# Optimization experiments

Measured on AMD Instinct MI355X. Metric: run time of the kernel, lower is better.

The kernel has to match this reference:

```python
import jax, jax.numpy as jnp
import numpy as np

B, T, D, H = 2, 2048, 1024, 16
Hd = D // H


def setup_inputs() -> dict:
    key = jax.random.key(0)
    ks = jax.random.split(key, 9)
    s = 1.0 / np.sqrt(D)
    return {
        "x": jax.random.normal(ks[0], (B, T, D), jnp.float32),
        "Wq": jax.random.normal(ks[1], (D, D), jnp.float32) * s,
        "bq": jax.random.normal(ks[2], (D,), jnp.float32) * 0.01,
        "Wk": jax.random.normal(ks[3], (D, D), jnp.float32) * s,
        "bk": jax.random.normal(ks[4], (D,), jnp.float32) * 0.01,
        "Wv": jax.random.normal(ks[5], (D, D), jnp.float32) * s,
        "bv": jax.random.normal(ks[6], (D,), jnp.float32) * 0.01,
        "Wo": jax.random.normal(ks[7], (D, D), jnp.float32) * s,
        "bo": jax.random.normal(ks[8], (D,), jnp.float32) * 0.01,
    }


def reference(x, Wq, bq, Wk, bk, Wv, bv, Wo, bo):
    # torch Linear: y = x @ W.T + b
    def proj(W, b):
        y = jnp.einsum('btd,ed->bte', x, W) + b          # [B,T,D]
        return y.reshape(B, T, H, Hd).transpose(0, 2, 1, 3)  # [B,H,T,Hd]
    q = proj(Wq, bq) / jnp.sqrt(jnp.asarray(Hd, x.dtype))
    k = proj(Wk, bk)
    v = proj(Wv, bv)
    scores = jnp.einsum('bhqd,bhkd->bhqk', q, k)         # [B,H,T,T]
    attn = jax.nn.softmax(scores, axis=-1)
    out = jnp.einsum('bhqk,bhkd->bhqd', attn, v)         # [B,H,T,Hd]
    out = out.transpose(0, 2, 1, 3).reshape(B, T, D)
    return jnp.einsum('btd,ed->bte', out, Wo) + bo
```

## Files before the change

kernel.cpp:

```cpp
#include <hip/hip_runtime.h>
#include <cmath>

typedef __attribute__((ext_vector_type(8))) short bf16x8;
typedef __attribute__((ext_vector_type(4))) float f32x4;

#define MFMA_BF16 __builtin_amdgcn_mfma_f32_16x16x32_bf16

__device__ __forceinline__ unsigned short f2b(float f) {
  union { float f; unsigned u; } v; v.f = f;
  unsigned r = (v.u + 0x7FFFu + ((v.u >> 16) & 1u)) >> 16;
  return (unsigned short)r;
}

__device__ __forceinline__ unsigned cvt_pk_bf16(float lo, float hi) {
  unsigned r;
  asm("v_cvt_pk_bf16_f32 %0, %1, %2" : "=v"(r) : "v"(lo), "v"(hi));
  return r;
}

__device__ __forceinline__ float fast_exp2(float x) {
  float r;
  asm("v_exp_f32 %0, %1" : "=v"(r) : "v"(x));
  return r;
}

__device__ __forceinline__ void gload_lds16(const void* g, void* l) {
  __builtin_amdgcn_global_load_lds(
      (const __attribute__((address_space(1))) void*)g,
      (__attribute__((address_space(3))) void*)l, 16, 0, 0);
}

__global__ __launch_bounds__(256) void cvt_all(
    const float* __restrict__ x, const float* __restrict__ Wq,
    const float* __restrict__ Wk, const float* __restrict__ Wv,
    const float* __restrict__ Wo,
    unsigned short* __restrict__ xb, unsigned short* __restrict__ wqb,
    unsigned short* __restrict__ wkb, unsigned short* __restrict__ wvb,
    unsigned short* __restrict__ wob) {
  int i = blockIdx.x * 256 + threadIdx.x;
  const float* src; unsigned short* dst; int off;
  if (i < 1048576)      { src = x;  dst = xb;  off = i; }
  else if (i < 1310720) { src = Wq; dst = wqb; off = i - 1048576; }
  else if (i < 1572864) { src = Wk; dst = wkb; off = i - 1310720; }
  else if (i < 1835008) { src = Wv; dst = wvb; off = i - 1572864; }
  else                  { src = Wo; dst = wob; off = i - 1835008; }
  float4 v = reinterpret_cast<const float4*>(src)[off];
  ushort4 o;
  o.x = f2b(v.x); o.y = f2b(v.y); o.z = f2b(v.z); o.w = f2b(v.w);
  reinterpret_cast<ushort4*>(dst)[off] = o;
}

__global__ __launch_bounds__(512, 4) void qkv_gemm(
    const unsigned short* __restrict__ X,
    const unsigned short* __restrict__ Wq, const unsigned short* __restrict__ Wk,
    const unsigned short* __restrict__ Wv,
    const float* __restrict__ bq, const float* __restrict__ bk,
    const float* __restrict__ bv,
    unsigned short* __restrict__ Qo, unsigned short* __restrict__ Ko,
    unsigned short* __restrict__ Vto) {
  __shared__ char smA[2][16384];
  __shared__ char smB[2][16384];
  const int tid = threadIdx.x, lane = tid & 63, wvid = tid >> 6;
  const int g = lane >> 4, l15 = lane & 15;
  const int wr = wvid >> 1, wc = wvid & 1;
  const int lin = blockIdx.y * 32 + blockIdx.x;
  const int xcd = lin & 7, j = lin >> 3;
  const int m_tile = (xcd >> 1) * 8 + (j & 7);
  const int bnall = (xcd & 1) * 12 + (j >> 3);
  const int m0 = m_tile * 128;
  const int wsel = bnall >> 3;
  const int n0 = (bnall & 7) * 128;
  const unsigned short* W = (wsel == 0) ? Wq : (wsel == 1) ? Wk : Wv;
  const float* bias = (wsel == 0) ? bq : (wsel == 1) ? bk : bv;

  f32x4 acc[2][4];
#pragma unroll
  for (int i = 0; i < 2; ++i)
#pragma unroll
    for (int j2 = 0; j2 < 4; ++j2) acc[i][j2] = (f32x4){0.f, 0.f, 0.f, 0.f};

#define QSTAGE(b, kt)                                                          \
  {                                                                            \
    _Pragma("unroll") for (int i = 0; i < 2; ++i) {                            \
      int c = (i * 8 + wvid) * 64 + lane;                                      \
      int row = c >> 3;                                                        \
      int cb = (c & 7) ^ (row & 7);                                            \
      gload_lds16(X + (size_t)(m0 + row) * 1024 + (kt) * 64 + cb * 8,          \
                  smA[b] + (i * 8 + wvid) * 1024);                             \
      gload_lds16(W + (size_t)(n0 + row) * 1024 + (kt) * 64 + cb * 8,          \
                  smB[b] + (i * 8 + wvid) * 1024);                             \
    }                                                                          \
  }

  QSTAGE(0, 0);
  int buf = 0;
  for (int kt = 0; kt < 16; ++kt) {
    __syncthreads();
    if (kt < 15) QSTAGE(buf ^ 1, kt + 1);
    bf16x8 af[2][2], bfr[4][2];
#pragma unroll
    for (int mi = 0; mi < 2; ++mi)
#pragma unroll
      for (int ks = 0; ks < 2; ++ks) {
        int rowa = wr * 32 + mi * 16 + l15;
        int addra = (rowa * 128 + ks * 64 + g * 16) ^ ((rowa & 7) << 4);
        af[mi][ks] = *(const bf16x8*)(smA[buf] + addra);
      }
#pragma unroll
    for (int ni = 0; ni < 4; ++ni)
#pragma unroll
      for (int ks = 0; ks < 2; ++ks) {
        int rowb = wc * 64 + ni * 16 + l15;
        int addrb = (rowb * 128 + ks * 64 + g * 16) ^ ((rowb & 7) << 4);
        bfr[ni][ks] = *(const bf16x8*)(smB[buf] + addrb);
      }
    __builtin_amdgcn_s_setprio(1);
#pragma unroll
    for (int ks = 0; ks < 2; ++ks)
#pragma unroll
      for (int mi = 0; mi < 2; ++mi)
#pragma unroll
        for (int ni = 0; ni < 4; ++ni)
          acc[mi][ni] = MFMA_BF16(af[mi][ks], bfr[ni][ks], acc[mi][ni], 0, 0, 0);
    __builtin_amdgcn_s_setprio(0);
    buf ^= 1;
  }

  const float qscale = (wsel == 0) ? 0.125f * 1.44269504f : 1.0f;
#pragma unroll
  for (int mi = 0; mi < 2; ++mi)
#pragma unroll
    for (int ni = 0; ni < 4; ++ni)
#pragma unroll
      for (int r = 0; r < 4; ++r) {
        int m = m0 + wr * 32 + mi * 16 + g * 4 + r;
        int n = n0 + wc * 64 + ni * 16 + l15;
        float v = (acc[mi][ni][r] + bias[n]) * qscale;
        int b = m >> 11, t = m & 2047;
        int h = n >> 6, hd = n & 63;
        unsigned short bv16 = f2b(v);
        if (wsel == 2)
          Vto[(((size_t)b * 16 + h) * 64 + hd) * 2048 + t] = bv16;
        else if (wsel == 1)
          Ko[(((size_t)b * 16 + h) * 2048 + t) * 64 + hd] = bv16;
        else
          Qo[(((size_t)b * 16 + h) * 2048 + t) * 64 + hd] = bv16;
      }
}

__global__ __launch_bounds__(512) void attn_kernel(
    const unsigned short* __restrict__ Qg, const unsigned short* __restrict__ Kg,
    const unsigned short* __restrict__ Vtg, unsigned short* __restrict__ Og) {
  __shared__ char smK[2][8192];
  __shared__ char smV[2][8192];
  __shared__ char smPT[8][2048];
  const int tid = threadIdx.x, lane = tid & 63, wvid = tid >> 6;
  const int g = lane >> 4, l15 = lane & 15;
  const int lin = blockIdx.y * 16 + blockIdx.x;
  const int wg = (lin & 7) * 64 + (lin >> 3);
  const int bx = wg & 15, bh = wg >> 4;
  const int q0 = bx * 128 + wvid * 16;
  const unsigned short* Qh = Qg + (size_t)bh * 2048 * 64;
  const unsigned short* Kh = Kg + (size_t)bh * 2048 * 64;
  const unsigned short* Vh = Vtg + (size_t)bh * 64 * 2048;

  bf16x8 qf[2];
#pragma unroll
  for (int ks = 0; ks < 2; ++ks)
    qf[ks] = *(const bf16x8*)(Qh + (size_t)(q0 + l15) * 64 + ks * 32 + g * 8);

  bf16x8 ones;
#pragma unroll
  for (int j = 0; j < 8; ++j) ones[j] = (short)0x3F80;

  f32x4 acc[4];
  f32x4 accL;
#pragma unroll
  for (int di = 0; di < 4; ++di) acc[di] = (f32x4){0.f, 0.f, 0.f, 0.f};
  accL = (f32x4){0.f, 0.f, 0.f, 0.f};
  float m = -1e30f;

#define STAGE(buf, kt)                                                         \
  {                                                                            \
    int c = wvid * 64 + lane;                                                  \
    int row = c >> 3;                                                          \
    int cb = (c & 7) ^ (row & 7);                                              \
    gload_lds16(Kh + (size_t)((kt) * 64 + row) * 64 + cb * 8,                  \
                smK[buf] + wvid * 1024);                                       \
    gload_lds16(Vh + (size_t)row * 2048 + (kt) * 64 + cb * 8,                  \
                smV[buf] + wvid * 1024);                                       \
  }

  STAGE(0, 0);
  __syncthreads();
  int buf = 0;
  char* P = smPT[wvid];

  for (int kt = 0; kt < 32; ++kt) {
    if (kt < 31) STAGE(buf ^ 1, kt + 1);

    f32x4 st[4];
#pragma unroll
    for (int ki = 0; ki < 4; ++ki) st[ki] = (f32x4){0.f, 0.f, 0.f, 0.f};
    __builtin_amdgcn_s_setprio(1);
#pragma unroll
    for (int ks = 0; ks < 2; ++ks)
#pragma unroll
      for (int ki = 0; ki < 4; ++ki) {
        int row = ki * 16 + l15;
        int addr = (row * 128 + ks * 64 + g * 16) ^ ((row & 7) << 4);
        bf16x8 kb = *(const bf16x8*)(smK[buf] + addr);
        st[ki] = MFMA_BF16(kb, qf[ks], st[ki], 0, 0, 0);
      }
    __builtin_amdgcn_s_setprio(0);

    float mx = -1e30f;
#pragma unroll
    for (int ki = 0; ki < 4; ++ki)
#pragma unroll
      for (int r = 0; r < 4; ++r) mx = fmaxf(mx, st[ki][r]);
    mx = fmaxf(mx, __shfl_xor(mx, 16, 64));
    mx = fmaxf(mx, __shfl_xor(mx, 32, 64));
    if (!__all(mx <= m + 8.f)) {
      float mnew = fmaxf(m, mx);
      float alpha = fast_exp2(m - mnew);
#pragma unroll
      for (int di = 0; di < 4; ++di) acc[di] *= alpha;
      accL *= alpha;
      m = mnew;
    }
#pragma unroll
    for (int ki = 0; ki < 4; ++ki) {
#pragma unroll
      for (int r = 0; r < 4; ++r) st[ki][r] = fast_exp2(st[ki][r] - m);
      uint2 w;
      w.x = cvt_pk_bf16(st[ki][0], st[ki][1]);
      w.y = cvt_pk_bf16(st[ki][2], st[ki][3]);
      int addr = (l15 * 128 + ki * 32 + g * 8) ^ ((l15 & 7) << 4);
      *(uint2*)(P + addr) = w;
    }

#pragma unroll
    for (int ks = 0; ks < 2; ++ks) {
      int paddr = (l15 * 128 + ks * 64 + g * 16) ^ ((l15 & 7) << 4);
      bf16x8 pb = *(const bf16x8*)(P + paddr);
      __builtin_amdgcn_s_setprio(1);
      accL = MFMA_BF16(ones, pb, accL, 0, 0, 0);
#pragma unroll
      for (int di = 0; di < 4; ++di) {
        int d = di * 16 + l15;
        int vaddr = (d * 128 + ks * 64 + g * 16) ^ ((d & 7) << 4);
        bf16x8 vb = *(const bf16x8*)(smV[buf] + vaddr);
        acc[di] = MFMA_BF16(vb, pb, acc[di], 0, 0, 0);
      }
      __builtin_amdgcn_s_setprio(0);
    }

    __syncthreads();
    buf ^= 1;
  }

  float inv = 1.0f / accL[0];
#pragma unroll
  for (int di = 0; di < 4; ++di) {
    uint2 w;
    w.x = cvt_pk_bf16(acc[di][0] * inv, acc[di][1] * inv);
    w.y = cvt_pk_bf16(acc[di][2] * inv, acc[di][3] * inv);
    int addr = (l15 * 128 + di * 32 + g * 8) ^ ((l15 & 7) << 4);
    *(uint2*)(P + addr) = w;
  }
  const int b = bh >> 4, h = bh & 15;
#pragma unroll
  for (int i = 0; i < 2; ++i) {
    int c = i * 64 + lane;
    int q = c >> 3, cb = c & 7;
    int addr = (q * 128 + cb * 16) ^ ((q & 7) << 4);
    uint4 v = *(const uint4*)(P + addr);
    int t = q0 + q;
    *(uint4*)(Og + ((size_t)(b * 2048 + t)) * 1024 + h * 64 + cb * 8) = v;
  }
}

__global__ __launch_bounds__(512, 4) void out_gemm(
    const unsigned short* __restrict__ A, const unsigned short* __restrict__ W,
    const float* __restrict__ bias, float* __restrict__ out) {
  __shared__ char smA[2][16384];
  __shared__ char smB[2][16384];
  const int tid = threadIdx.x, lane = tid & 63, wvid = tid >> 6;
  const int g = lane >> 4, l15 = lane & 15;
  const int wr = wvid >> 1, wc = wvid & 1;
  const int lin = blockIdx.y * 32 + blockIdx.x;
  const int xcd = lin & 7, j = lin >> 3;
  const int m0 = (xcd * 4 + (j & 3)) * 128;
  const int n0 = (j >> 2) * 128;

  f32x4 acc[2][4];
#pragma unroll
  for (int i = 0; i < 2; ++i)
#pragma unroll
    for (int j2 = 0; j2 < 4; ++j2) acc[i][j2] = (f32x4){0.f, 0.f, 0.f, 0.f};

#define OSTAGE(b, kt)                                                          \
  {                                                                            \
    _Pragma("unroll") for (int i = 0; i < 2; ++i) {                            \
      int c = (i * 8 + wvid) * 64 + lane;                                      \
      int row = c >> 3;                                                        \
      int cb = (c & 7) ^ (row & 7);                                            \
      gload_lds16(A + (size_t)(m0 + row) * 1024 + (kt) * 64 + cb * 8,          \
                  smA[b] + (i * 8 + wvid) * 1024);                             \
      gload_lds16(W + (size_t)(n0 + row) * 1024 + (kt) * 64 + cb * 8,          \
                  smB[b] + (i * 8 + wvid) * 1024);                             \
    }                                                                          \
  }

  OSTAGE(0, 0);
  int buf = 0;
  for (int kt = 0; kt < 16; ++kt) {
    __syncthreads();
    if (kt < 15) OSTAGE(buf ^ 1, kt + 1);
    bf16x8 af[2][2], bfr[4][2];
#pragma unroll
    for (int mi = 0; mi < 2; ++mi)
#pragma unroll
      for (int ks = 0; ks < 2; ++ks) {
        int rowa = wr * 32 + mi * 16 + l15;
        int addra = (rowa * 128 + ks * 64 + g * 16) ^ ((rowa & 7) << 4);
        af[mi][ks] = *(const bf16x8*)(smA[buf] + addra);
      }
#pragma unroll
    for (int ni = 0; ni < 4; ++ni)
#pragma unroll
      for (int ks = 0; ks < 2; ++ks) {
        int rowb = wc * 64 + ni * 16 + l15;
        int addrb = (rowb * 128 + ks * 64 + g * 16) ^ ((rowb & 7) << 4);
        bfr[ni][ks] = *(const bf16x8*)(smB[buf] + addrb);
      }
    __builtin_amdgcn_s_setprio(1);
#pragma unroll
    for (int ks = 0; ks < 2; ++ks)
#pragma unroll
      for (int mi = 0; mi < 2; ++mi)
#pragma unroll
        for (int ni = 0; ni < 4; ++ni)
          acc[mi][ni] = MFMA_BF16(af[mi][ks], bfr[ni][ks], acc[mi][ni], 0, 0, 0);
    __builtin_amdgcn_s_setprio(0);
    buf ^= 1;
  }

#pragma unroll
  for (int mi = 0; mi < 2; ++mi)
#pragma unroll
    for (int ni = 0; ni < 4; ++ni)
#pragma unroll
      for (int r = 0; r < 4; ++r) {
        int mm = m0 + wr * 32 + mi * 16 + g * 4 + r;
        int nn = n0 + wc * 64 + ni * 16 + l15;
        out[(size_t)mm * 1024 + nn] = acc[mi][ni][r] + bias[nn];
      }
}

extern "C" void kernel_launch(void* const* d_in, const int* in_sizes, int n_in,
                              void* d_out, int out_size, void* d_ws, size_t ws_size,
                              hipStream_t stream) {
  const float* x = (const float*)d_in[0];
  const float* Wq = (const float*)d_in[1];
  const float* bq = (const float*)d_in[2];
  const float* Wk = (const float*)d_in[3];
  const float* bk = (const float*)d_in[4];
  const float* Wv = (const float*)d_in[5];
  const float* bv = (const float*)d_in[6];
  const float* Wo = (const float*)d_in[7];
  const float* bo = (const float*)d_in[8];
  float* out = (float*)d_out;
  char* ws = (char*)d_ws;

  unsigned short* xb = (unsigned short*)(ws + 0);
  unsigned short* Ob = (unsigned short*)(ws + 0);
  unsigned short* wqb = (unsigned short*)(ws + 8388608);
  unsigned short* wkb = (unsigned short*)(ws + 10485760);
  unsigned short* wvb = (unsigned short*)(ws + 12582912);
  unsigned short* wob = (unsigned short*)(ws + 14680064);
  unsigned short* Qb = (unsigned short*)(ws + 16777216);
  unsigned short* Kb = (unsigned short*)(ws + 25165824);
  unsigned short* Vtb = (unsigned short*)(ws + 33554432);

  hipLaunchKernelGGL(cvt_all, dim3(8192), dim3(256), 0, stream,
                     x, Wq, Wk, Wv, Wo, xb, wqb, wkb, wvb, wob);
  hipLaunchKernelGGL(qkv_gemm, dim3(32, 24), dim3(512), 0, stream, xb, wqb, wkb, wvb,
                     bq, bk, bv, Qb, Kb, Vtb);
  hipLaunchKernelGGL(attn_kernel, dim3(16, 32), dim3(512), 0, stream, Qb, Kb, Vtb, Ob);
  hipLaunchKernelGGL(out_gemm, dim3(32, 8), dim3(512), 0, stream, Ob, wob, bo, out);
}
```

Baseline: 123.2 us.

## Give each attention wave two 16-row query tiles to reuse K/V fragments

The attention block shrinks from 8 waves to 4, and each wave now handles 32 query rows as two 16-row sub-tiles. Every K and V fragment read from LDS feeds two MFMAs instead of one. This halves LDS read traffic per MFMA, and each wave issues twice the K/V staging loads. In exchange, register pressure roughly doubles for accumulators and scores, and there are fewer waves per block to hide latency.

```diff
diff --git a/kernel.cpp b/kernel.cpp
--- a/kernel.cpp
+++ b/kernel.cpp
@@ -148,47 +148,54 @@
       }
 }
 
-__global__ __launch_bounds__(512) void attn_kernel(
+__global__ __launch_bounds__(256, 2) void attn_kernel(
     const unsigned short* __restrict__ Qg, const unsigned short* __restrict__ Kg,
     const unsigned short* __restrict__ Vtg, unsigned short* __restrict__ Og) {
   __shared__ char smK[2][8192];
   __shared__ char smV[2][8192];
-  __shared__ char smPT[8][2048];
+  __shared__ char smPT[4][4096];
   const int tid = threadIdx.x, lane = tid & 63, wvid = tid >> 6;
   const int g = lane >> 4, l15 = lane & 15;
   const int lin = blockIdx.y * 16 + blockIdx.x;
   const int wg = (lin & 7) * 64 + (lin >> 3);
   const int bx = wg & 15, bh = wg >> 4;
-  const int q0 = bx * 128 + wvid * 16;
+  const int q0 = bx * 128 + wvid * 32;
   const unsigned short* Qh = Qg + (size_t)bh * 2048 * 64;
   const unsigned short* Kh = Kg + (size_t)bh * 2048 * 64;
   const unsigned short* Vh = Vtg + (size_t)bh * 64 * 2048;
 
-  bf16x8 qf[2];
-#pragma unroll
-  for (int ks = 0; ks < 2; ++ks)
-    qf[ks] = *(const bf16x8*)(Qh + (size_t)(q0 + l15) * 64 + ks * 32 + g * 8);
+  bf16x8 qf[2][2];
+#pragma unroll
+  for (int qi = 0; qi < 2; ++qi)
+#pragma unroll
+    for (int ks = 0; ks < 2; ++ks)
+      qf[qi][ks] = *(const bf16x8*)(Qh + (size_t)(q0 + qi * 16 + l15) * 64 + ks * 32 + g * 8);
 
   bf16x8 ones;
 #pragma unroll
   for (int j = 0; j < 8; ++j) ones[j] = (short)0x3F80;
 
-  f32x4 acc[4];
-  f32x4 accL;
-#pragma unroll
-  for (int di = 0; di < 4; ++di) acc[di] = (f32x4){0.f, 0.f, 0.f, 0.f};
-  accL = (f32x4){0.f, 0.f, 0.f, 0.f};
-  float m = -1e30f;
+  f32x4 acc[4][2];
+  f32x4 accL[2];
+#pragma unroll
+  for (int di = 0; di < 4; ++di)
+#pragma unroll
+    for (int qi = 0; qi < 2; ++qi) acc[di][qi] = (f32x4){0.f, 0.f, 0.f, 0.f};
+  accL[0] = (f32x4){0.f, 0.f, 0.f, 0.f};
+  accL[1] = (f32x4){0.f, 0.f, 0.f, 0.f};
+  float m[2] = {-1e30f, -1e30f};
 
 #define STAGE(buf, kt)                                                         \
   {                                                                            \
-    int c = wvid * 64 + lane;                                                  \
-    int row = c >> 3;                                                          \
-    int cb = (c & 7) ^ (row & 7);                                              \
-    gload_lds16(Kh + (size_t)((kt) * 64 + row) * 64 + cb * 8,                  \
-                smK[buf] + wvid * 1024);                                       \
-    gload_lds16(Vh + (size_t)row * 2048 + (kt) * 64 + cb * 8,                  \
-                smV[buf] + wvid * 1024);                                       \
+    _Pragma("unroll") for (int i = 0; i < 2; ++i) {                            \
+      int c = (i * 4 + wvid) * 64 + lane;                                      \
+      int row = c >> 3;                                                        \
+      int cb = (c & 7) ^ (row & 7);                                            \
+      gload_lds16(Kh + (size_t)((kt) * 64 + row) * 64 + cb * 8,                \
+                  smK[buf] + (i * 4 + wvid) * 1024);                           \
+      gload_lds16(Vh + (size_t)row * 2048 + (kt) * 64 + cb * 8,                \
+                  smV[buf] + (i * 4 + wvid) * 1024);                           \
+    }                                                                          \
   }
 
   STAGE(0, 0);
@@ -199,9 +206,11 @@
   for (int kt = 0; kt < 32; ++kt) {
     if (kt < 31) STAGE(buf ^ 1, kt + 1);
 
-    f32x4 st[4];
-#pragma unroll
-    for (int ki = 0; ki < 4; ++ki) st[ki] = (f32x4){0.f, 0.f, 0.f, 0.f};
+    f32x4 st[4][2];
+#pragma unroll
+    for (int ki = 0; ki < 4; ++ki)
+#pragma unroll
+      for (int qi = 0; qi < 2; ++qi) st[ki][qi] = (f32x4){0.f, 0.f, 0.f, 0.f};
     __builtin_amdgcn_s_setprio(1);
 #pragma unroll
     for (int ks = 0; ks < 2; ++ks)
@@ -210,48 +219,63 @@
         int row = ki * 16 + l15;
         int addr = (row * 128 + ks * 64 + g * 16) ^ ((row & 7) << 4);
         bf16x8 kb = *(const bf16x8*)(smK[buf] + addr);
-        st[ki] = MFMA_BF16(kb, qf[ks], st[ki], 0, 0, 0);
+#pragma unroll
+        for (int qi = 0; qi < 2; ++qi)
+          st[ki][qi] = MFMA_BF16(kb, qf[qi][ks], st[ki][qi], 0, 0, 0);
       }
     __builtin_amdgcn_s_setprio(0);
 
-    float mx = -1e30f;
-#pragma unroll
-    for (int ki = 0; ki < 4; ++ki)
-#pragma unroll
-      for (int r = 0; r < 4; ++r) mx = fmaxf(mx, st[ki][r]);
-    mx = fmaxf(mx, __shfl_xor(mx, 16, 64));
-    mx = fmaxf(mx, __shfl_xor(mx, 32, 64));
-    if (!__all(mx <= m + 8.f)) {
-      float mnew = fmaxf(m, mx);
-      float alpha = fast_exp2(m - mnew);
-#pragma unroll
-      for (int di = 0; di < 4; ++di) acc[di] *= alpha;
-      accL *= alpha;
-      m = mnew;
+#pragma unroll
+    for (int qi = 0; qi < 2; ++qi) {
+      float mx = -1e30f;
+#pragma unroll
+      for (int ki = 0; ki < 4; ++ki)
+#pragma unroll
+        for (int r = 0; r < 4; ++r) mx = fmaxf(mx, st[ki][qi][r]);
+      mx = fmaxf(mx, __shfl_xor(mx, 16, 64));
+      mx = fmaxf(mx, __shfl_xor(mx, 32, 64));
+      if (!__all(mx <= m[qi] + 8.f)) {
+        float mnew = fmaxf(m[qi], mx);
+        float alpha = fast_exp2(m[qi] - mnew);
+#pragma unroll
+        for (int di = 0; di < 4; ++di) acc[di][qi] *= alpha;
+        accL[qi] *= alpha;
+        m[qi] = mnew;
+      }
+#pragma unroll
+      for (int ki = 0; ki < 4; ++ki) {
+#pragma unroll
+        for (int r = 0; r < 4; ++r) st[ki][qi][r] = fast_exp2(st[ki][qi][r] - m[qi]);
+        uint2 w;
+        w.x = cvt_pk_bf16(st[ki][qi][0], st[ki][qi][1]);
+        w.y = cvt_pk_bf16(st[ki][qi][2], st[ki][qi][3]);
+        int q = qi * 16 + l15;
+        int addr = (q * 128 + ki * 32 + g * 8) ^ ((q & 7) << 4);
+        *(uint2*)(P + addr) = w;
+      }
     }
-#pragma unroll
-    for (int ki = 0; ki < 4; ++ki) {
-#pragma unroll
-      for (int r = 0; r < 4; ++r) st[ki][r] = fast_exp2(st[ki][r] - m);
-      uint2 w;
-      w.x = cvt_pk_bf16(st[ki][0], st[ki][1]);
-      w.y = cvt_pk_bf16(st[ki][2], st[ki][3]);
-      int addr = (l15 * 128 + ki * 32 + g * 8) ^ ((l15 & 7) << 4);
-      *(uint2*)(P + addr) = w;
-    }
 
 #pragma unroll
     for (int ks = 0; ks < 2; ++ks) {
-      int paddr = (l15 * 128 + ks * 64 + g * 16) ^ ((l15 & 7) << 4);
-      bf16x8 pb = *(const bf16x8*)(P + paddr);
+      bf16x8 pb[2];
+#pragma unroll
+      for (int qi = 0; qi < 2; ++qi) {
+        int q = qi * 16 + l15;
+        int paddr = (q * 128 + ks * 64 + g * 16) ^ ((q & 7) << 4);
+        pb[qi] = *(const bf16x8*)(P + paddr);
+      }
       __builtin_amdgcn_s_setprio(1);
-      accL = MFMA_BF16(ones, pb, accL, 0, 0, 0);
+#pragma unroll
+      for (int qi = 0; qi < 2; ++qi)
+        accL[qi] = MFMA_BF16(ones, pb[qi], accL[qi], 0, 0, 0);
 #pragma unroll
       for (int di = 0; di < 4; ++di) {
         int d = di * 16 + l15;
         int vaddr = (d * 128 + ks * 64 + g * 16) ^ ((d & 7) << 4);
         bf16x8 vb = *(const bf16x8*)(smV[buf] + vaddr);
-        acc[di] = MFMA_BF16(vb, pb, acc[di], 0, 0, 0);
+#pragma unroll
+        for (int qi = 0; qi < 2; ++qi)
+          acc[di][qi] = MFMA_BF16(vb, pb[qi], acc[di][qi], 0, 0, 0);
       }
       __builtin_amdgcn_s_setprio(0);
     }
@@ -260,18 +284,21 @@
     buf ^= 1;
   }
 
-  float inv = 1.0f / accL[0];
-#pragma unroll
-  for (int di = 0; di < 4; ++di) {
-    uint2 w;
-    w.x = cvt_pk_bf16(acc[di][0] * inv, acc[di][1] * inv);
-    w.y = cvt_pk_bf16(acc[di][2] * inv, acc[di][3] * inv);
-    int addr = (l15 * 128 + di * 32 + g * 8) ^ ((l15 & 7) << 4);
-    *(uint2*)(P + addr) = w;
-  }
+  float inv[2] = {1.f / accL[0][0], 1.f / accL[1][0]};
+#pragma unroll
+  for (int qi = 0; qi < 2; ++qi)
+#pragma unroll
+    for (int di = 0; di < 4; ++di) {
+      uint2 w;
+      w.x = cvt_pk_bf16(acc[di][qi][0] * inv[qi], acc[di][qi][1] * inv[qi]);
+      w.y = cvt_pk_bf16(acc[di][qi][2] * inv[qi], acc[di][qi][3] * inv[qi]);
+      int q = qi * 16 + l15;
+      int addr = (q * 128 + di * 32 + g * 8) ^ ((q & 7) << 4);
+      *(uint2*)(P + addr) = w;
+    }
   const int b = bh >> 4, h = bh & 15;
 #pragma unroll
-  for (int i = 0; i < 2; ++i) {
+  for (int i = 0; i < 4; ++i) {
     int c = i * 64 + lane;
     int q = c >> 3, cb = c & 7;
     int addr = (q * 128 + cb * 16) ^ ((q & 7) << 4);
@@ -388,6 +415,6 @@
                      x, Wq, Wk, Wv, Wo, xb, wqb, wkb, wvb, wob);
   hipLaunchKernelGGL(qkv_gemm, dim3(32, 24), dim3(512), 0, stream, xb, wqb, wkb, wvb,
                      bq, bk, bv, Qb, Kb, Vtb);
-  hipLaunchKernelGGL(attn_kernel, dim3(16, 32), dim3(512), 0, stream, Qb, Kb, Vtb, Ob);
+  hipLaunchKernelGGL(attn_kernel, dim3(16, 32), dim3(256), 0, stream, Qb, Kb, Vtb, Ob);
   hipLaunchKernelGGL(out_gemm, dim3(32, 8), dim3(512), 0, stream, Ob, wob, bo, out);
 }
```

After: 127.0 us. 1.03x slower.
